# Kernel optimization log

Hardware: AMD Instinct MI355X
Metric: run time of the kernel (lower is better)

## Reference

```python
import jax, jax.numpy as jnp
import numpy as np

N_HEADS = 16

def setup_inputs() -> dict:
    key = jax.random.key(0)
    k1, k2, k3 = jax.random.split(key, 3)
    B, T, C = 4, 2048, 1024
    x = jax.random.normal(k1, (B, T, C), dtype=jnp.float32)
    w_qkv = jax.random.normal(k2, (C, 3 * C), dtype=jnp.float32) * (1.0 / np.sqrt(C))
    w_out = jax.random.normal(k3, (C, C), dtype=jnp.float32) * (1.0 / np.sqrt(C))
    return {"x": x, "w_qkv": w_qkv, "w_out": w_out}

def reference(x, w_qkv, w_out):
    B, T, C = x.shape
    H = N_HEADS
    d_k = C // H
    qkv = x @ w_qkv                       # (B,T,3C)
    q, k, v = jnp.split(qkv, 3, axis=-1)
    # (B,H,T,d_k)
    q = q.reshape(B, T, H, d_k).transpose(0, 2, 1, 3)
    k = k.reshape(B, T, H, d_k).transpose(0, 2, 1, 3)
    v = v.reshape(B, T, H, d_k).transpose(0, 2, 1, 3)
    scale = 1.0 / np.sqrt(d_k)
    scores = jnp.einsum('bhqd,bhkd->bhqk', q, k) * scale  # (B,H,T,T)
    causal = jnp.triu(jnp.ones((T, T), dtype=bool), k=1)  # True = ignore
    scores = jnp.where(causal, -jnp.inf, scores)
    weights = jax.nn.softmax(scores, axis=-1)
    out = jnp.einsum('bhqk,bhkd->bhqd', weights, v)       # (B,H,T,d_k)
    out = out.transpose(0, 2, 1, 3).reshape(B, T, C)
    return out @ w_out
```

## Files before the change

kernel.cpp:

```cpp
#include <hip/hip_runtime.h>
#include <hip/hip_bf16.h>
#include <stdint.h>
#include <math.h>

typedef __bf16 bf16;
typedef __bf16 bf16x4 __attribute__((ext_vector_type(4)));
typedef __bf16 bf16x8 __attribute__((ext_vector_type(8)));
typedef float f32x4 __attribute__((ext_vector_type(4)));

#define BB 4
#define TT 2048
#define CC 1024
#define HH 16
#define DK 64

__device__ __forceinline__ void gl_lds16(const void* gsrc, void* ldst) {
    __builtin_amdgcn_global_load_lds(
        (__attribute__((address_space(1))) void*)(void*)(gsrc),
        (__attribute__((address_space(3))) void*)(ldst),
        16, 0, 0);
}

__device__ __forceinline__ void bar() {
    asm volatile("" ::: "memory");
    __builtin_amdgcn_s_barrier();
    asm volatile("" ::: "memory");
}
#define VMCNT(N) asm volatile("s_waitcnt vmcnt(" #N ")" ::: "memory")

__global__ __launch_bounds__(256) void prep(
    const float* __restrict__ x, const float* __restrict__ wq,
    const float* __restrict__ wo, bf16* __restrict__ xbf,
    bf16* __restrict__ wqT, bf16* __restrict__ woT) {
    __shared__ bf16 tile[32][33];
    const int bid = blockIdx.x, tid = threadIdx.x;
    if (bid < 4096) {
        const int i = (bid * 256 + tid) * 8;
        const f32x4 a = *(const f32x4*)(x + i);
        const f32x4 b = *(const f32x4*)(x + i + 4);
        bf16x8 o;
#pragma unroll
        for (int j = 0; j < 4; ++j) { o[j] = (bf16)a[j]; o[j + 4] = (bf16)b[j]; }
        *(bf16x8*)(xbf + i) = o;
        return;
    }
    const float* in;
    bf16* out;
    int R, C, c0, r0;
    if (bid < 7168) {
        const int tb = bid - 4096;
        in = wq; out = wqT; R = 1024; C = 3072;
        c0 = (tb % 96) * 32; r0 = (tb / 96) * 32;
    } else {
        const int tb = bid - 7168;
        in = wo; out = woT; R = 1024; C = 1024;
        c0 = (tb % 32) * 32; r0 = (tb / 32) * 32;
    }
    const int tx = tid & 31, ty = tid >> 5;
#pragma unroll
    for (int i = 0; i < 32; i += 8)
        tile[ty + i][tx] = (bf16)in[(size_t)(r0 + ty + i) * C + c0 + tx];
    __syncthreads();
#pragma unroll
    for (int i = 0; i < 32; i += 8)
        out[(size_t)(c0 + ty + i) * R + r0 + tx] = tile[tx][ty + i];
}

template <int EPI>
__global__ __launch_bounds__(512, 2) void gemm256(
    const bf16* __restrict__ A, const bf16* __restrict__ Bt,
    void* __restrict__ Cq, bf16* __restrict__ Kh, bf16* __restrict__ Vt,
    int M, int N, int K) {
    __shared__ bf16 As[2][256 * 64];
    __shared__ bf16 Bs[2][256 * 64];
    const int tid = threadIdx.x;
    const int w = tid >> 6, l = tid & 63;
    const int wm = w >> 2, wn = w & 3;
    const int lm = l & 15, lq = l >> 4;
    const int m0 = blockIdx.y * 256, n0 = blockIdx.x * 256;

    const int srow_a = w * 8 + (l >> 3);
    const int srow_b = (w & 3) * 8 + (w >> 2) * 64 + (l >> 3);
    const int csw = ((l & 7) ^ (l >> 3)) * 8;
    const bf16* agl = A + (size_t)(m0 + srow_a) * K + csw;
    const bf16* bgl = Bt + (size_t)(n0 + srow_b) * K + csw;
    const int wa = w * 8;
    const int wb = (w & 3) * 8 + (w >> 2) * 64;

    int aoff[2], boff[2];
#pragma unroll
    for (int ks = 0; ks < 2; ++ks) {
        const int sl = (ks * 4 + lq) ^ (lm & 7);
        aoff[ks] = (wm * 128 + lm) * 64 + sl * 8;
        boff[ks] = (wn * 64 + lm) * 64 + sl * 8;
    }

    f32x4 acc[8][4] = {};
    bf16x8 af[4][2], bfA[2][2], bfB[2][2];

#define STGA(R, DSTA, KOFF) gl_lds16(agl + (size_t)(R) * K + (KOFF), (DSTA) + (wa + (R)) * 64)
#define STGB(R, DSTB, KOFF) gl_lds16(bgl + (size_t)(R) * K + (KOFF), (DSTB) + (wb + (R)) * 64)
#define LDA(MIH, SRC)                                                          \
    _Pragma("unroll") for (int mi = 0; mi < 4; ++mi)                           \
    _Pragma("unroll") for (int ks = 0; ks < 2; ++ks)                           \
        af[mi][ks] = *(const bf16x8*)((SRC) + aoff[ks] + ((MIH) * 4 + mi) * 1024);
#define LDB(BF, NIH, SRC)                                                      \
    _Pragma("unroll") for (int ni = 0; ni < 2; ++ni)                           \
    _Pragma("unroll") for (int ks = 0; ks < 2; ++ks)                           \
        BF[ni][ks] = *(const bf16x8*)((SRC) + boff[ks] + ((NIH) * 2 + ni) * 1024);
#define QMFMA(MIH, NIH, BF)                                                    \
    __builtin_amdgcn_s_setprio(1);                                             \
    _Pragma("unroll") for (int ks = 0; ks < 2; ++ks)                           \
    _Pragma("unroll") for (int mi = 0; mi < 4; ++mi)                           \
    _Pragma("unroll") for (int ni = 0; ni < 2; ++ni)                           \
        acc[(MIH) * 4 + mi][(NIH) * 2 + ni] =                                  \
            __builtin_amdgcn_mfma_f32_16x16x32_bf16(                           \
                af[mi][ks], BF[ni][ks], acc[(MIH) * 4 + mi][(NIH) * 2 + ni],   \
                0, 0, 0);                                                      \
    __builtin_amdgcn_s_setprio(0);

    bf16* A0 = &As[0][0]; bf16* A1 = &As[1][0];
    bf16* B0 = &Bs[0][0]; bf16* B1 = &Bs[1][0];
    const int NT = K >> 6;

    STGA(0, A0, 0); STGA(128, A0, 0);
    STGB(0, B0, 0); STGB(128, B0, 0);
    STGB(32, B0, 0); STGB(160, B0, 0);
    STGA(64, A0, 0); STGA(192, A0, 0);
    VMCNT(4); bar();

    for (int t = 0; t < NT - 1; ++t) {
        const int bb = t & 1;
        const bf16* Ac = bb ? A1 : A0; const bf16* Bc = bb ? B1 : B0;
        bf16* An = bb ? A0 : A1;       bf16* Bn = bb ? B0 : B1;
        const int k1 = (t + 1) << 6;
        LDA(0, Ac); LDB(bfA, 0, Bc);
        STGA(0, An, k1); STGA(128, An, k1);
        bar();
        QMFMA(0, 0, bfA);
        VMCNT(4); bar();
        LDB(bfB, 1, Bc);
        STGB(0, Bn, k1); STGB(128, Bn, k1);
        bar();
        QMFMA(0, 1, bfB);
        VMCNT(4); bar();
        LDA(1, Ac);
        STGB(32, Bn, k1); STGB(160, Bn, k1);
        bar();
        QMFMA(1, 1, bfB);
        bar();
        STGA(64, An, k1); STGA(192, An, k1);
        bar();
        QMFMA(1, 0, bfA);
        VMCNT(4); bar();
    }
    {
        const int bb = (NT - 1) & 1;
        const bf16* Ac = bb ? A1 : A0; const bf16* Bc = bb ? B1 : B0;
        LDA(0, Ac); LDB(bfA, 0, Bc);
        bar(); QMFMA(0, 0, bfA); VMCNT(2); bar();
        LDB(bfB, 1, Bc);
        bar(); QMFMA(0, 1, bfB); VMCNT(0); bar();
        LDA(1, Ac);
        bar(); QMFMA(1, 1, bfB); bar();
        QMFMA(1, 0, bfA);
    }

    if (EPI == 0) {
#pragma unroll
        for (int mi = 0; mi < 8; ++mi) {
            const int row = m0 + wm * 128 + mi * 16 + lq * 4;
#pragma unroll
            for (int ni = 0; ni < 4; ++ni) {
                const int col = n0 + wn * 64 + ni * 16 + lm;
#pragma unroll
                for (int r = 0; r < 4; ++r)
                    ((float*)Cq)[(size_t)(row + r) * N + col] = acc[mi][ni][r];
            }
        }
    } else {
        bf16* Q = (bf16*)Cq;
#pragma unroll
        for (int ni = 0; ni < 4; ++ni) {
            const int c = n0 + wn * 64 + ni * 16 + lm;
            const int part = c >> 10;
            const int h = (c & 1023) >> 6;
            const int d = c & 63;
#pragma unroll
            for (int mi = 0; mi < 8; ++mi) {
                const int rowg = m0 + wm * 128 + mi * 16 + lq * 4;
#pragma unroll
                for (int r = 0; r < 4; ++r) {
                    const int rg = rowg + r;
                    const int b = rg >> 11, t = rg & 2047;
                    const bf16 v = (bf16)acc[mi][ni][r];
                    if (part == 0)
                        Q[((size_t)(b * HH + h) * TT + t) * DK + d] = v;
                    else if (part == 1)
                        Kh[((size_t)(b * HH + h) * TT + t) * DK + d] = v;
                    else
                        Vt[((size_t)(b * HH + h) * DK + d) * TT + t] = v;
                }
            }
        }
    }
#undef STGA
#undef STGB
#undef LDA
#undef LDB
#undef QMFMA
}

#define PAD 72
__global__ __launch_bounds__(256, 3) void attn_kernel(
    const bf16* __restrict__ Qh, const bf16* __restrict__ Kh,
    const bf16* __restrict__ Vt, bf16* __restrict__ O) {
    __shared__ bf16 Ks[2][64 * PAD];
    __shared__ bf16 Vs[2][64 * PAD];
    __shared__ bf16 Ps[64 * PAD];
    const int tid = threadIdx.x, w = tid >> 6, l = tid & 63;
    const int lm = l & 15, lq = l >> 4;
    const int id = blockIdx.x;
    const int xcd = id & 7;
    const int rest = id >> 3;
    const int bh = xcd + 8 * (rest >> 4);
    const int p = rest & 15;
    const int b = bh >> 4, h = bh & 15;
    const bf16* Qb = Qh + (size_t)bh * TT * DK;
    const bf16* Kb = Kh + (size_t)bh * TT * DK;
    const bf16* Vb = Vt + (size_t)bh * DK * TT;
    const int srow = tid >> 3, scol = (tid & 7) * 8;

    const float smul = 0.125f * 1.44269504088896340736f;
    const int qts[2] = {p, 31 - p};

    bf16x8 kreg[2], vreg[2];
#pragma unroll
    for (int i = 0; i < 2; ++i) {
        kreg[i] = *(const bf16x8*)(Kb + (size_t)(srow + i * 32) * DK + scol);
        vreg[i] = *(const bf16x8*)(Vb + (size_t)(srow + i * 32) * TT + scol);
    }
    int buf = 0;

#pragma unroll
    for (int half = 0; half < 2; ++half) {
        const int qt = qts[half];
        const int q0 = qt * 64;
        const int qg = q0 + w * 16 + lm;

        bf16x8 qf[2];
#pragma unroll
        for (int ks = 0; ks < 2; ++ks)
            qf[ks] = *(const bf16x8*)(Qb + (size_t)(q0 + w * 16 + lm) * DK +
                                      ks * 32 + lq * 8);

        f32x4 oacc[4] = {};
        float lrun = 0.f;

        for (int kt = 0; kt <= qt; ++kt) {
#pragma unroll
            for (int i = 0; i < 2; ++i) {
                *(bf16x8*)(Ks[buf] + (srow + i * 32) * PAD + scol) = kreg[i];
                *(bf16x8*)(Vs[buf] + (srow + i * 32) * PAD + scol) = vreg[i];
            }
            __syncthreads();

            {
                int nkt = -1;
                if (kt < qt) nkt = kt + 1;
                else if (half == 0) nkt = 0;
                if (nkt >= 0) {
#pragma unroll
                    for (int i = 0; i < 2; ++i) {
                        kreg[i] = *(const bf16x8*)(
                            Kb + (size_t)(nkt * 64 + srow + i * 32) * DK + scol);
                        vreg[i] = *(const bf16x8*)(
                            Vb + (size_t)(srow + i * 32) * TT + nkt * 64 + scol);
                    }
                }
            }

            f32x4 st[4] = {};
#pragma unroll
            for (int ks = 0; ks < 2; ++ks) {
#pragma unroll
                for (int nb = 0; nb < 4; ++nb) {
                    const bf16x8 kf = *(const bf16x8*)(Ks[buf] + (nb * 16 + lm) * PAD +
                                                       ks * 32 + lq * 8);
                    st[nb] = __builtin_amdgcn_mfma_f32_16x16x32_bf16(
                        kf, qf[ks], st[nb], 0, 0, 0);
                }
            }

            const bool diag = (kt == qt);
#pragma unroll
            for (int nb = 0; nb < 4; ++nb) {
                bf16x4 pk;
#pragma unroll
                for (int r = 0; r < 4; ++r) {
                    float arg = fmaf(st[nb][r], smul, -20.f);
                    if (diag) {
                        const int keyg = kt * 64 + nb * 16 + lq * 4 + r;
                        if (keyg > qg) arg = -1e30f;
                    }
                    const float pv = exp2f(arg);
                    lrun += pv;
                    pk[r] = (bf16)pv;
                }
                *(bf16x4*)(Ps + (w * 16 + lm) * PAD + nb * 16 + lq * 4) = pk;
            }

#pragma unroll
            for (int ks = 0; ks < 2; ++ks) {
                const bf16x8 pf =
                    *(const bf16x8*)(Ps + (w * 16 + lm) * PAD + ks * 32 + lq * 8);
#pragma unroll
                for (int ni = 0; ni < 4; ++ni) {
                    const bf16x8 vf = *(const bf16x8*)(Vs[buf] + (ni * 16 + lm) * PAD +
                                                       ks * 32 + lq * 8);
                    oacc[ni] = __builtin_amdgcn_mfma_f32_16x16x32_bf16(
                        pf, vf, oacc[ni], 0, 0, 0);
                }
            }
            buf ^= 1;
        }

        lrun += __shfl_xor(lrun, 16);
        lrun += __shfl_xor(lrun, 32);
        float linv[4];
#pragma unroll
        for (int r = 0; r < 4; ++r) linv[r] = 1.0f / __shfl(lrun, lq * 4 + r);
#pragma unroll
        for (int ni = 0; ni < 4; ++ni) {
            const int col = h * 64 + ni * 16 + lm;
#pragma unroll
            for (int r = 0; r < 4; ++r) {
                const int t = q0 + w * 16 + lq * 4 + r;
                O[((size_t)(b * TT + t)) * CC + col] = (bf16)(oacc[ni][r] * linv[r]);
            }
        }
    }
}

extern "C" void kernel_launch(void* const* d_in, const int* in_sizes, int n_in,
                              void* d_out, int out_size, void* d_ws, size_t ws_size,
                              hipStream_t stream) {
    const float* x = (const float*)d_in[0];
    const float* w_qkv = (const float*)d_in[1];
    const float* w_out = (const float*)d_in[2];

    char* ws = (char*)d_ws;
    const size_t M1 = (size_t)1 << 20;
    bf16* Qh = (bf16*)(ws);
    bf16* Kh = (bf16*)(ws + 16 * M1);
    bf16* Vt = (bf16*)(ws + 32 * M1);
    bf16* Ob = (bf16*)(ws + 48 * M1);
    bf16* wqkvT = (bf16*)(ws + 64 * M1);
    bf16* woutT = (bf16*)(ws + 70 * M1);
    bf16* xbf = (bf16*)(ws + 72 * M1);

    prep<<<8192, 256, 0, stream>>>(x, w_qkv, w_out, xbf, wqkvT, woutT);
    gemm256<1><<<dim3(3072 / 256, 8192 / 256), 512, 0, stream>>>(
        xbf, wqkvT, Qh, Kh, Vt, 8192, 3072, 1024);
    attn_kernel<<<1024, 256, 0, stream>>>(Qh, Kh, Vt, Ob);
    gemm256<0><<<dim3(1024 / 256, 8192 / 256), 512, 0, stream>>>(
        Ob, woutT, (float*)d_out, nullptr, nullptr, 8192, 1024, 1024);
}
```

Before: 279.2 us.

## Reschedule GEMM main loop with inline LDS reads, early A prefetch, XCD swizzle

```diff
diff --git a/kernel.cpp b/kernel.cpp
--- a/kernel.cpp
+++ b/kernel.cpp
@@ -27,6 +27,15 @@
     asm volatile("" ::: "memory");
 }
 #define VMCNT(N) asm volatile("s_waitcnt vmcnt(" #N ")" ::: "memory")
+#define LGKM0()                                          \
+    do {                                                 \
+        asm volatile("s_waitcnt lgkmcnt(0)" ::: "memory"); \
+        __builtin_amdgcn_sched_barrier(0);               \
+    } while (0)
+
+__device__ __forceinline__ void ds_read16(bf16x8& r, uint32_t addr) {
+    asm volatile("ds_read_b128 %0, %1" : "=v"(r) : "v"(addr));
+}
 
 __global__ __launch_bounds__(256) void prep(
     const float* __restrict__ x, const float* __restrict__ wq,
@@ -70,14 +79,18 @@
 __global__ __launch_bounds__(512, 2) void gemm256(
     const bf16* __restrict__ A, const bf16* __restrict__ Bt,
     void* __restrict__ Cq, bf16* __restrict__ Kh, bf16* __restrict__ Vt,
-    int M, int N, int K) {
+    int M, int N, int K, int nxg) {
     __shared__ bf16 As[2][256 * 64];
     __shared__ bf16 Bs[2][256 * 64];
     const int tid = threadIdx.x;
     const int w = tid >> 6, l = tid & 63;
     const int wm = w >> 2, wn = w & 3;
     const int lm = l & 15, lq = l >> 4;
-    const int m0 = blockIdx.y * 256, n0 = blockIdx.x * 256;
+
+    const int nwg = gridDim.x;
+    const int sw = (blockIdx.x & 7) * (nwg >> 3) + (blockIdx.x >> 3);
+    const int bx = sw % nxg, by = sw / nxg;
+    const int m0 = by * 256, n0 = bx * 256;
 
     const int srow_a = w * 8 + (l >> 3);
     const int srow_b = (w & 3) * 8 + (w >> 2) * 64 + (l >> 3);
@@ -87,27 +100,23 @@
     const int wa = w * 8;
     const int wb = (w & 3) * 8 + (w >> 2) * 64;
 
-    int aoff[2], boff[2];
+    uint32_t aoffB[2], boffB[2];
 #pragma unroll
     for (int ks = 0; ks < 2; ++ks) {
         const int sl = (ks * 4 + lq) ^ (lm & 7);
-        aoff[ks] = (wm * 128 + lm) * 64 + sl * 8;
-        boff[ks] = (wn * 64 + lm) * 64 + sl * 8;
-    }
+        aoffB[ks] = (uint32_t)(((wm * 128 + lm) * 64 + sl * 8) * 2);
+        boffB[ks] = (uint32_t)(((wn * 64 + lm) * 64 + sl * 8) * 2);
+    }
+    const uint32_t AsU0 = (uint32_t)(uintptr_t)&As[0][0];
+    const uint32_t AsU1 = (uint32_t)(uintptr_t)&As[1][0];
+    const uint32_t BsU0 = (uint32_t)(uintptr_t)&Bs[0][0];
+    const uint32_t BsU1 = (uint32_t)(uintptr_t)&Bs[1][0];
 
     f32x4 acc[8][4] = {};
-    bf16x8 af[4][2], bfA[2][2], bfB[2][2];
+    bf16x8 af[4][2], be[2][2], bl[2][2];
 
 #define STGA(R, DSTA, KOFF) gl_lds16(agl + (size_t)(R) * K + (KOFF), (DSTA) + (wa + (R)) * 64)
 #define STGB(R, DSTB, KOFF) gl_lds16(bgl + (size_t)(R) * K + (KOFF), (DSTB) + (wb + (R)) * 64)
-#define LDA(MIH, SRC)                                                          \
-    _Pragma("unroll") for (int mi = 0; mi < 4; ++mi)                           \
-    _Pragma("unroll") for (int ks = 0; ks < 2; ++ks)                           \
-        af[mi][ks] = *(const bf16x8*)((SRC) + aoff[ks] + ((MIH) * 4 + mi) * 1024);
-#define LDB(BF, NIH, SRC)                                                      \
-    _Pragma("unroll") for (int ni = 0; ni < 2; ++ni)                           \
-    _Pragma("unroll") for (int ks = 0; ks < 2; ++ks)                           \
-        BF[ni][ks] = *(const bf16x8*)((SRC) + boff[ks] + ((NIH) * 2 + ni) * 1024);
 #define QMFMA(MIH, NIH, BF)                                                    \
     __builtin_amdgcn_s_setprio(1);                                             \
     _Pragma("unroll") for (int ks = 0; ks < 2; ++ks)                           \
@@ -127,43 +136,54 @@
     STGB(0, B0, 0); STGB(128, B0, 0);
     STGB(32, B0, 0); STGB(160, B0, 0);
     STGA(64, A0, 0); STGA(192, A0, 0);
+    STGA(0, A1, 64); STGA(128, A1, 64);
     VMCNT(4); bar();
 
-    for (int t = 0; t < NT - 1; ++t) {
+    for (int t = 0; t < NT; ++t) {
         const int bb = t & 1;
-        const bf16* Ac = bb ? A1 : A0; const bf16* Bc = bb ? B1 : B0;
-        bf16* An = bb ? A0 : A1;       bf16* Bn = bb ? B0 : B1;
-        const int k1 = (t + 1) << 6;
-        LDA(0, Ac); LDB(bfA, 0, Bc);
-        STGA(0, An, k1); STGA(128, An, k1);
+        const uint32_t Ar = bb ? AsU1 : AsU0, Br = bb ? BsU1 : BsU0;
+        bf16* An = bb ? A0 : A1;  bf16* Bn = bb ? B0 : B1;
+        bf16* Aw = bb ? A1 : A0;
+        const int k1 = (t + 1) << 6, k2 = (t + 2) << 6;
+        const bool sN = (t + 1 < NT), sN2 = (t + 2 < NT);
+
+#pragma unroll
+        for (int mi = 0; mi < 4; ++mi)
+#pragma unroll
+            for (int ks = 0; ks < 2; ++ks)
+                ds_read16(af[mi][ks], Ar + aoffB[ks] + mi * 2048);
+#pragma unroll
+        for (int ni = 0; ni < 2; ++ni)
+#pragma unroll
+            for (int ks = 0; ks < 2; ++ks)
+                ds_read16(be[ni][ks], Br + boffB[ks] + ni * 2048);
+        if (sN) { STGB(0, Bn, k1); STGB(128, Bn, k1); }
+        LGKM0();
+#pragma unroll
+        for (int ni = 0; ni < 2; ++ni)
+#pragma unroll
+            for (int ks = 0; ks < 2; ++ks)
+                ds_read16(bl[ni][ks], Br + boffB[ks] + (2 + ni) * 2048);
+        QMFMA(0, 0, be);
         bar();
-        QMFMA(0, 0, bfA);
-        VMCNT(4); bar();
-        LDB(bfB, 1, Bc);
-        STGB(0, Bn, k1); STGB(128, Bn, k1);
+        if (sN) { STGB(32, Bn, k1); STGB(160, Bn, k1); }
+        LGKM0();
+        QMFMA(0, 1, bl);
+        if (sN) { VMCNT(6); } else { VMCNT(0); }
         bar();
-        QMFMA(0, 1, bfB);
-        VMCNT(4); bar();
-        LDA(1, Ac);
-        STGB(32, Bn, k1); STGB(160, Bn, k1);
+#pragma unroll
+        for (int mi = 0; mi < 4; ++mi)
+#pragma unroll
+            for (int ks = 0; ks < 2; ++ks)
+                ds_read16(af[mi][ks], Ar + aoffB[ks] + 8192 + mi * 2048);
+        if (sN) { STGA(64, An, k1); STGA(192, An, k1); }
+        LGKM0();
+        QMFMA(1, 1, bl);
+        if (sN2) { STGA(0, Aw, k2); STGA(128, Aw, k2); }
+        QMFMA(1, 0, be);
+        if (sN2) { VMCNT(4); }
+        else if (sN) { VMCNT(2); }
         bar();
-        QMFMA(1, 1, bfB);
-        bar();
-        STGA(64, An, k1); STGA(192, An, k1);
-        bar();
-        QMFMA(1, 0, bfA);
-        VMCNT(4); bar();
-    }
-    {
-        const int bb = (NT - 1) & 1;
-        const bf16* Ac = bb ? A1 : A0; const bf16* Bc = bb ? B1 : B0;
-        LDA(0, Ac); LDB(bfA, 0, Bc);
-        bar(); QMFMA(0, 0, bfA); VMCNT(2); bar();
-        LDB(bfB, 1, Bc);
-        bar(); QMFMA(0, 1, bfB); VMCNT(0); bar();
-        LDA(1, Ac);
-        bar(); QMFMA(1, 1, bfB); bar();
-        QMFMA(1, 0, bfA);
     }
 
     if (EPI == 0) {
@@ -206,8 +226,6 @@
     }
 #undef STGA
 #undef STGB
-#undef LDA
-#undef LDB
 #undef QMFMA
 }
 
@@ -360,9 +378,9 @@
     bf16* xbf = (bf16*)(ws + 72 * M1);
 
     prep<<<8192, 256, 0, stream>>>(x, w_qkv, w_out, xbf, wqkvT, woutT);
-    gemm256<1><<<dim3(3072 / 256, 8192 / 256), 512, 0, stream>>>(
-        xbf, wqkvT, Qh, Kh, Vt, 8192, 3072, 1024);
+    gemm256<1><<<384, 512, 0, stream>>>(
+        xbf, wqkvT, Qh, Kh, Vt, 8192, 3072, 1024, 12);
     attn_kernel<<<1024, 256, 0, stream>>>(Qh, Kh, Vt, Ob);
-    gemm256<0><<<dim3(1024 / 256, 8192 / 256), 512, 0, stream>>>(
-        Ob, woutT, (float*)d_out, nullptr, nullptr, 8192, 1024, 1024);
-}
+    gemm256<0><<<128, 512, 0, stream>>>(
+        Ob, woutT, (float*)d_out, nullptr, nullptr, 8192, 1024, 1024, 4);
+}
```

After: 279.7 us. No clear change (+0.2%).

## Reuse idle K buffer for P, raise attention occupancy, smaller-tile output GEMM

Applied to the files above, without the earlier changes.

```diff
diff --git a/kernel.cpp b/kernel.cpp
--- a/kernel.cpp
+++ b/kernel.cpp
@@ -211,13 +211,92 @@
 #undef QMFMA
 }
 
+template <int EPI>
+__global__ __launch_bounds__(256) void gemm_bt(
+    const bf16* __restrict__ A, const bf16* __restrict__ Bt,
+    void* __restrict__ Cq, bf16* __restrict__ Kh, bf16* __restrict__ Vt,
+    int M, int N, int K) {
+    __shared__ bf16 As[128 * 32];
+    __shared__ bf16 Bs[128 * 32];
+    const int tid = threadIdx.x;
+    const int w = tid >> 6, l = tid & 63;
+    const int wm = w >> 1, wn = w & 1;
+    const int m0 = blockIdx.y * 128, n0 = blockIdx.x * 128;
+    const int lr4 = l >> 2, lc4 = (l & 3) * 8;
+    const int lm = l & 15, lq = l >> 4;
+
+    f32x4 acc[4][4] = {};
+
+    for (int k0 = 0; k0 < K; k0 += 32) {
+#pragma unroll
+        for (int i = 0; i < 2; ++i) {
+            const int j = w * 2 + i;
+            gl_lds16(A + (size_t)(m0 + j * 16 + lr4) * K + k0 + lc4, As + j * 512);
+            gl_lds16(Bt + (size_t)(n0 + j * 16 + lr4) * K + k0 + lc4, Bs + j * 512);
+        }
+        __syncthreads();
+        bf16x8 af[4], bfr[4];
+#pragma unroll
+        for (int mi = 0; mi < 4; ++mi)
+            af[mi] = *(const bf16x8*)(As + (wm * 64 + mi * 16 + lm) * 32 + lq * 8);
+#pragma unroll
+        for (int ni = 0; ni < 4; ++ni)
+            bfr[ni] = *(const bf16x8*)(Bs + (wn * 64 + ni * 16 + lm) * 32 + lq * 8);
+#pragma unroll
+        for (int mi = 0; mi < 4; ++mi)
+#pragma unroll
+            for (int ni = 0; ni < 4; ++ni)
+                acc[mi][ni] = __builtin_amdgcn_mfma_f32_16x16x32_bf16(
+                    af[mi], bfr[ni], acc[mi][ni], 0, 0, 0);
+        __syncthreads();
+    }
+
+    if (EPI == 0) {
+#pragma unroll
+        for (int mi = 0; mi < 4; ++mi) {
+            const int row = m0 + wm * 64 + mi * 16 + lq * 4;
+#pragma unroll
+            for (int ni = 0; ni < 4; ++ni) {
+                const int col = n0 + wn * 64 + ni * 16 + lm;
+#pragma unroll
+                for (int r = 0; r < 4; ++r)
+                    ((float*)Cq)[(size_t)(row + r) * N + col] = acc[mi][ni][r];
+            }
+        }
+    } else {
+        bf16* Q = (bf16*)Cq;
+#pragma unroll
+        for (int ni = 0; ni < 4; ++ni) {
+            const int c = n0 + wn * 64 + ni * 16 + lm;
+            const int part = c >> 10;
+            const int h = (c & 1023) >> 6;
+            const int d = c & 63;
+#pragma unroll
+            for (int mi = 0; mi < 4; ++mi) {
+                const int rowg = m0 + wm * 64 + mi * 16 + lq * 4;
+#pragma unroll
+                for (int r = 0; r < 4; ++r) {
+                    const int rg = rowg + r;
+                    const int b = rg >> 11, t = rg & 2047;
+                    const bf16 v = (bf16)acc[mi][ni][r];
+                    if (part == 0)
+                        Q[((size_t)(b * HH + h) * TT + t) * DK + d] = v;
+                    else if (part == 1)
+                        Kh[((size_t)(b * HH + h) * TT + t) * DK + d] = v;
+                    else
+                        Vt[((size_t)(b * HH + h) * DK + d) * TT + t] = v;
+                }
+            }
+        }
+    }
+}
+
 #define PAD 72
-__global__ __launch_bounds__(256, 3) void attn_kernel(
+__global__ __launch_bounds__(256, 4) void attn_kernel(
     const bf16* __restrict__ Qh, const bf16* __restrict__ Kh,
     const bf16* __restrict__ Vt, bf16* __restrict__ O) {
     __shared__ bf16 Ks[2][64 * PAD];
     __shared__ bf16 Vs[2][64 * PAD];
-    __shared__ bf16 Ps[64 * PAD];
     const int tid = threadIdx.x, w = tid >> 6, l = tid & 63;
     const int lm = l & 15, lq = l >> 4;
     const int id = blockIdx.x;
@@ -230,6 +309,7 @@
     const bf16* Kb = Kh + (size_t)bh * TT * DK;
     const bf16* Vb = Vt + (size_t)bh * DK * TT;
     const int srow = tid >> 3, scol = (tid & 7) * 8;
+    const int prow = w * 8 + (lm & 7) + ((lm >> 3) << 5);
 
     const float smul = 0.125f * 1.44269504088896340736f;
     const int qts[2] = {p, 31 - p};
@@ -264,6 +344,8 @@
                 *(bf16x8*)(Vs[buf] + (srow + i * 32) * PAD + scol) = vreg[i];
             }
             __syncthreads();
+
+            bf16* Pp = Ks[buf ^ 1];
 
             {
                 int nkt = -1;
@@ -281,6 +363,7 @@
             }
 
             f32x4 st[4] = {};
+            __builtin_amdgcn_s_setprio(1);
 #pragma unroll
             for (int ks = 0; ks < 2; ++ks) {
 #pragma unroll
@@ -291,6 +374,7 @@
                         kf, qf[ks], st[nb], 0, 0, 0);
                 }
             }
+            __builtin_amdgcn_s_setprio(0);
 
             const bool diag = (kt == qt);
 #pragma unroll
@@ -307,13 +391,14 @@
                     lrun += pv;
                     pk[r] = (bf16)pv;
                 }
-                *(bf16x4*)(Ps + (w * 16 + lm) * PAD + nb * 16 + lq * 4) = pk;
-            }
-
+                *(bf16x4*)(Pp + prow * PAD + nb * 16 + lq * 4) = pk;
+            }
+
+            __builtin_amdgcn_s_setprio(1);
 #pragma unroll
             for (int ks = 0; ks < 2; ++ks) {
                 const bf16x8 pf =
-                    *(const bf16x8*)(Ps + (w * 16 + lm) * PAD + ks * 32 + lq * 8);
+                    *(const bf16x8*)(Pp + prow * PAD + ks * 32 + lq * 8);
 #pragma unroll
                 for (int ni = 0; ni < 4; ++ni) {
                     const bf16x8 vf = *(const bf16x8*)(Vs[buf] + (ni * 16 + lm) * PAD +
@@ -322,6 +407,7 @@
                         pf, vf, oacc[ni], 0, 0, 0);
                 }
             }
+            __builtin_amdgcn_s_setprio(0);
             buf ^= 1;
         }
 
@@ -363,6 +449,6 @@
     gemm256<1><<<dim3(3072 / 256, 8192 / 256), 512, 0, stream>>>(
         xbf, wqkvT, Qh, Kh, Vt, 8192, 3072, 1024);
     attn_kernel<<<1024, 256, 0, stream>>>(Qh, Kh, Vt, Ob);
-    gemm256<0><<<dim3(1024 / 256, 8192 / 256), 512, 0, stream>>>(
+    gemm_bt<0><<<dim3(1024 / 128, 8192 / 128), 256, 0, stream>>>(
         Ob, woutT, (float*)d_out, nullptr, nullptr, 8192, 1024, 1024);
 }
```

Measured after the change: 274.3 us. About the same (-1.8%).
